# Performance work log

Hardware: AMD Instinct MI355X
Metric: run time of the kernel (lower is better)

Reference implementation:

```python
import jax, jax.numpy as jnp
import numpy as np
import math

B, S, E, H = 2, 2048, 1024, 16
D = E // H  # d_attn = 64
SCALE = 1.0 / math.sqrt(D)


def setup_inputs() -> dict:
    key = jax.random.key(0)
    ks = jax.random.split(key, 5)
    std = 0.02
    return {
        "q": jax.random.normal(ks[0], (B, S, E), dtype=jnp.float32),
        "Wq": jax.random.normal(ks[1], (E, H * D), dtype=jnp.float32) * std,
        "Wk": jax.random.normal(ks[2], (E, H * D), dtype=jnp.float32) * std,
        "Wv": jax.random.normal(ks[3], (E, H * D), dtype=jnp.float32) * std,
        "Wo": jax.random.normal(ks[4], (H * D, E), dtype=jnp.float32) * std,
        "gamma": jnp.ones((H,), dtype=jnp.float32),
    }


def reference(q, Wq, Wk, Wv, Wo, gamma):
    Bq, Sq, _ = q.shape
    # projections -> [B, H, S, D]
    qh = (q @ Wq).reshape(Bq, Sq, H, D).transpose(0, 2, 1, 3)
    kh = (q @ Wk).reshape(Bq, Sq, H, D).transpose(0, 2, 1, 3)
    vh = (q @ Wv).reshape(Bq, Sq, H, D).transpose(0, 2, 1, 3)
    # RBF distance scores: ||q||^2 - 2 q.k + ||k||^2, clamped at 0
    q_norm = jnp.sum(qh * qh, axis=-1, keepdims=True)          # [B,H,S,1]
    k_norm = jnp.sum(kh * kh, axis=-1, keepdims=True)          # [B,H,S,1]
    qk = jnp.einsum("bhsd,bhtd->bhst", qh, kh)                # [B,H,S,S]
    dist = jnp.maximum(q_norm - 2.0 * qk + jnp.swapaxes(k_norm, -2, -1), 0.0)
    scores = jnp.exp(-gamma[None, :, None, None] * SCALE * dist)
    # source: masked_fill(causal_mask == 0, 0) with mask = triu(ones, 1)
    # -> scores kept only on the STRICT upper triangle (faithful to source)
    mask = jnp.triu(jnp.ones((Sq, Sq), dtype=bool), k=1)
    scores = jnp.where(mask, scores, 0.0)
    out = jnp.einsum("bhst,bhtd->bhsd", scores, vh)            # [B,H,S,D]
    out = out.transpose(0, 2, 1, 3).reshape(Bq, Sq, H * D)
    return out @ Wo
```

## Files before the change

### kernel.cpp

```cpp
#include <hip/hip_runtime.h>
#include <stdint.h>

#define SCALE 0.125f
#define GSL_C 0.180336880111f

typedef short s16x4 __attribute__((ext_vector_type(4)));
typedef short s16x8 __attribute__((ext_vector_type(8)));
typedef float f32x4 __attribute__((ext_vector_type(4)));
typedef float f32x16 __attribute__((ext_vector_type(16)));

__device__ __forceinline__ unsigned short f2bf(float x){
  union { float f; unsigned int u; } v; v.f = x;
  unsigned int r = v.u + 0x7fffu + ((v.u >> 16) & 1u);
  return (unsigned short)(r >> 16);
}
__device__ __forceinline__ float bf2f(unsigned short u){
  union { unsigned int u; float f; } v; v.u = ((unsigned int)u) << 16;
  return v.f;
}
__device__ __forceinline__ f32x4 mfma16(s16x8 a, s16x8 b, f32x4 c){
  return __builtin_amdgcn_mfma_f32_16x16x32_bf16(a, b, c, 0, 0, 0);
}
__device__ __forceinline__ f32x16 mfma32(s16x8 a, s16x8 b, f32x16 c){
  return __builtin_amdgcn_mfma_f32_32x32x16_bf16(a, b, c, 0, 0, 0);
}
__device__ __forceinline__ void gld_lds16(const void* g, void* l){
  __builtin_amdgcn_global_load_lds(
      (const __attribute__((address_space(1))) unsigned int*)g,
      (__attribute__((address_space(3))) unsigned int*)l, 16, 0, 0);
}
__device__ __forceinline__ unsigned int cvtpk(float lo, float hi){
  unsigned int r;
  asm("v_cvt_pk_bf16_f32 %0, %1, %2" : "=v"(r) : "v"(lo), "v"(hi));
  return r;
}
__device__ __forceinline__ void plswap(unsigned int &a, unsigned int &b){
  asm("v_permlane32_swap_b32 %0, %1" : "+v"(a), "+v"(b));
}

__global__ __launch_bounds__(256) void prep_kernel(const float* __restrict__ in,
    unsigned short* __restrict__ out,
    const float* __restrict__ W0, const float* __restrict__ W1,
    const float* __restrict__ W2, const float* __restrict__ W3,
    unsigned short* __restrict__ Wt){
  int bid = blockIdx.x;
  int tid = threadIdx.x;
  if (bid < 2048){
    int i = bid*256 + tid;
    const float4* p = (const float4*)in + (size_t)i*2;
    float4 a = p[0], b = p[1];
    unsigned short t[8] = {f2bf(a.x),f2bf(a.y),f2bf(a.z),f2bf(a.w),
                           f2bf(b.x),f2bf(b.y),f2bf(b.z),f2bf(b.w)};
    *(s16x8*)(out + (size_t)i*8) = *(const s16x8*)t;
  } else {
    int idx = bid - 2048;
    int z = idx >> 8, rem = idx & 255;
    int k0 = (rem & 15)*64, n0 = (rem >> 4)*64;
    const float* src = (z==0)?W0:(z==1)?W1:(z==2)?W2:W3;
    unsigned short* dst = Wt + (size_t)z*1048576;
    __shared__ unsigned short tile[64*72];
    int r = tid>>2, c = (tid&3)*16;
    const float* p = src + (size_t)(k0+r)*1024 + n0 + c;
    #pragma unroll
    for (int j=0;j<16;j++) tile[r*72 + c + j] = f2bf(p[j]);
    __syncthreads();
    int n = tid>>2, kc = (tid&3)*16;
    unsigned short o[16];
    #pragma unroll
    for (int j=0;j<16;j++) o[j] = tile[(kc+j)*72 + n];
    *(s16x8*)&dst[(size_t)(n0+n)*1024 + k0 + kc]     = *(const s16x8*)o;
    *(s16x8*)&dst[(size_t)(n0+n)*1024 + k0 + kc + 8] = *(const s16x8*)(o+8);
  }
}

__global__ __launch_bounds__(512) void gemm_proj(const unsigned short* __restrict__ A,
    const unsigned short* __restrict__ Bt, unsigned short* __restrict__ outH,
    unsigned short* __restrict__ VtG,
    float* __restrict__ qn, float* __restrict__ kn, const float* __restrict__ gamma){
  __shared__ short As[3][4096];
  __shared__ short Bs[3][4096];
  int tid = threadIdx.x;
  int w = tid>>6, l = tid&63;
  int lm = l & 15, hi = l >> 4;
  int wr = w>>1, wc = w&1;
  int m0 = blockIdx.x*128, n0 = blockIdx.y*128;

  const unsigned short* Bz = Bt + (size_t)(n0>>10)*1048576;
  int bn0 = n0 & 1023;

  f32x4 acc[2][4];
  #pragma unroll
  for (int r=0;r<2;r++)
    #pragma unroll
    for (int c=0;c<4;c++){ f32x4 z = {0.f,0.f,0.f,0.f}; acc[r][c] = z; }

  int srow = w*16 + (l>>2);
  int schk = ((l&3) ^ ((l>>3)&3))*8;
  const unsigned short* gA = A  + (size_t)(m0  + srow)*1024 + schk;
  const unsigned short* gB = Bz + (size_t)(bn0 + srow)*1024 + schk;

  int ch = (hi ^ ((lm>>1)&3))*8;

  gld_lds16(gA,      &As[0][w*512]);
  gld_lds16(gB,      &Bs[0][w*512]);
  gld_lds16(gA + 32, &As[1][w*512]);
  gld_lds16(gB + 32, &Bs[1][w*512]);

  const int NKT = 32;
  int cur = 0;
  for (int kt=0; kt<NKT; ++kt){
    if (kt+2 < NKT){
      int wb = cur + 2; if (wb >= 3) wb -= 3;
      gld_lds16(gA + (size_t)(kt+2)*32, &As[wb][w*512]);
      gld_lds16(gB + (size_t)(kt+2)*32, &Bs[wb][w*512]);
    }
    if (kt < NKT-2)       asm volatile("s_waitcnt vmcnt(4)" ::: "memory");
    else if (kt == NKT-2) asm volatile("s_waitcnt vmcnt(2)" ::: "memory");
    else                  asm volatile("s_waitcnt vmcnt(0)" ::: "memory");
    __builtin_amdgcn_s_barrier();

    const short* cA = &As[cur][0];
    const short* cB = &Bs[cur][0];
    s16x8 af[2], bfv[4];
    #pragma unroll
    for (int r=0;r<2;r++)
      af[r]  = *(const s16x8*)(cA + (wr*32 + r*16 + lm)*32 + ch);
    #pragma unroll
    for (int c=0;c<4;c++)
      bfv[c] = *(const s16x8*)(cB + (wc*64 + c*16 + lm)*32 + ch);
    __builtin_amdgcn_s_setprio(1);
    #pragma unroll
    for (int r=0;r<2;r++)
      #pragma unroll
      for (int c=0;c<4;c++)
        acc[r][c] = mfma16(af[r], bfv[c], acc[r][c]);
    __builtin_amdgcn_s_setprio(0);
    __builtin_amdgcn_s_barrier();
    cur = (cur + 1 < 3) ? cur + 1 : 0;
  }

  int z = n0 >> 10;
  if (z == 2){
    short* tb = (w < 4) ? (&As[0][0] + w*2048) : (&Bs[0][0] + (w-4)*2048);
    #pragma unroll
    for (int r=0;r<2;r++)
      #pragma unroll
      for (int c=0;c<4;c++){
        unsigned short t4[4] = {f2bf(acc[r][c][0]), f2bf(acc[r][c][1]),
                                f2bf(acc[r][c][2]), f2bf(acc[r][c][3])};
        *(s16x4*)(tb + (c*16 + lm)*32 + r*16 + hi*4) = *(const s16x4*)t4;
      }
    int bq = m0 >> 11;
    int hq = (bn0 >> 6) + wc;
    int bh = bq*16 + hq;
    int t0w = (m0 & 2047) + wr*32;
    unsigned short* vt = VtG + (size_t)bh*131072;
    #pragma unroll
    for (int it=0; it<4; ++it){
      int d = (l>>2) + it*16;
      int tl = (l&3)*8;
      s16x8 vv = *(const s16x8*)(tb + d*32 + tl);
      *(s16x8*)(vt + (size_t)d*2048 + t0w + tl) = vv;
    }
  } else {
    unsigned short* oz = outH + (size_t)z*4194304;
    #pragma unroll
    for (int r=0;r<2;r++){
      #pragma unroll
      for (int i=0;i<4;i++){
        int m = m0 + wr*32 + r*16 + hi*4 + i;
        int bq = m >> 11, sq = m & 2047;
        float nrm = 0.f;
        #pragma unroll
        for (int c=0;c<4;c++){
          int nn = bn0 + wc*64 + c*16 + lm;
          int hq = nn >> 6, dq = nn & 63;
          int bh = bq*16 + hq;
          unsigned short bv = f2bf(acc[r][c][i]);
          oz[((size_t)bh*2048 + sq)*64 + dq] = bv;
          float vf = bf2f(bv);
          nrm = fmaf(vf, vf, nrm);
        }
        nrm += __shfl_xor(nrm, 1);
        nrm += __shfl_xor(nrm, 2);
        nrm += __shfl_xor(nrm, 4);
        nrm += __shfl_xor(nrm, 8);
        if (lm == 0){
          int hq = (bn0 + wc*64) >> 6;
          float gsl_h = gamma[hq] * GSL_C;
          float* dst = z ? kn : qn;
          dst[(size_t)(bq*16 + hq)*2048 + sq] = nrm * gsl_h;
        }
      }
    }
  }
}

__global__ __launch_bounds__(512) void gemm_out(const unsigned short* __restrict__ A,
    const unsigned short* __restrict__ Bt, float* __restrict__ outF){
  __shared__ short As[16384];
  __shared__ short Bs[8192];
  int tid = threadIdx.x;
  int w = tid>>6, l = tid&63;
  int lm = l & 15, hi = l >> 4;
  int wr = w>>1, wc = w&1;
  int m0 = blockIdx.x*128, n0 = blockIdx.y*64;

  f32x4 acc[2][2];
  #pragma unroll
  for (int r=0;r<2;r++)
    #pragma unroll
    for (int c=0;c<2;c++){ f32x4 z = {0.f,0.f,0.f,0.f}; acc[r][c] = z; }

  int rsub = l>>3, csw = ((l&7) ^ (l>>3))*8;
  const unsigned short* gA = A  + (size_t)(m0 + w*16 + rsub)*1024 + csw;
  const unsigned short* gB = Bt + (size_t)(n0 + w*8  + rsub)*1024 + csw;

  int ch0 = ((hi)     ^ (lm&7))*8;
  int ch1 = ((4 + hi) ^ (lm&7))*8;

  gld_lds16(gA,        As + w*1024);
  gld_lds16(gA + 8192, As + w*1024 + 512);
  gld_lds16(gB,        Bs + w*512);
  __syncthreads();

  const int NKT = 16;
  int buf = 0;
  for (int kt=0; kt<NKT; ++kt){
    if (kt+1 < NKT){
      const unsigned short* a = gA + (size_t)(kt+1)*64;
      const unsigned short* b = gB + (size_t)(kt+1)*64;
      gld_lds16(a,        As + (buf^1)*8192 + w*1024);
      gld_lds16(a + 8192, As + (buf^1)*8192 + w*1024 + 512);
      gld_lds16(b,        Bs + (buf^1)*4096 + w*512);
    }
    const short* curA = As + buf*8192;
    const short* curB = Bs + buf*4096;
    s16x8 af[2][2], bfv[2][2];
    #pragma unroll
    for (int r=0;r<2;r++){
      int ro = (wr*32 + r*16 + lm)*64;
      af[r][0] = *(const s16x8*)(curA + ro + ch0);
      af[r][1] = *(const s16x8*)(curA + ro + ch1);
    }
    #pragma unroll
    for (int c=0;c<2;c++){
      int ro = (wc*32 + c*16 + lm)*64;
      bfv[c][0] = *(const s16x8*)(curB + ro + ch0);
      bfv[c][1] = *(const s16x8*)(curB + ro + ch1);
    }
    __builtin_amdgcn_s_setprio(1);
    #pragma unroll
    for (int s=0;s<2;s++)
      #pragma unroll
      for (int r=0;r<2;r++)
        #pragma unroll
        for (int c=0;c<2;c++)
          acc[r][c] = mfma16(af[r][s], bfv[c][s], acc[r][c]);
    __builtin_amdgcn_s_setprio(0);
    __syncthreads();
    buf ^= 1;
  }

  #pragma unroll
  for (int r=0;r<2;r++)
    #pragma unroll
    for (int c=0;c<2;c++)
      #pragma unroll
      for (int i=0;i<4;i++){
        int m = m0 + wr*32 + r*16 + hi*4 + i;
        int n = n0 + wc*32 + c*16 + lm;
        outF[(size_t)m*1024 + n] = acc[r][c][i];
      }
}

#define JOB(si,ts,te,buf,zm) ((unsigned int)((si)|((ts)<<4)|((te)<<10)|((buf)<<16)|((zm)<<18)))
__device__ const unsigned int JOBS[32] = {
  JOB(0,0,11,0,0),   JOB(5,10,21,0,0),  JOB(0,22,32,2,0),  JOB(1,12,22,1,0),
  JOB(2,4,14,0,0),   JOB(6,22,32,1,2),  JOB(2,23,32,2,0),  JOB(7,14,23,0,0),
  JOB(0,11,22,1,0),  JOB(5,21,32,1,2),  JOB(1,2,12,0,0),   JOB(1,22,32,2,0),
  JOB(6,12,22,0,0),  JOB(2,14,23,1,0),  JOB(3,6,15,0,0),   JOB(7,23,32,1,2),
  JOB(11,22,32,0,3), JOB(3,24,32,2,0),  JOB(4,8,16,0,0),   JOB(4,16,24,1,0),
  JOB(4,24,32,2,0),  JOB(8,16,24,0,0),  JOB(3,15,24,1,0),  JOB(8,24,32,1,2),
  JOB(15,30,32,0,3), JOB(14,28,32,0,3), JOB(10,20,26,0,0), JOB(10,26,32,1,2),
  JOB(13,26,32,0,3), JOB(9,18,25,0,0),  JOB(9,25,32,1,2),  JOB(12,24,32,0,3)
};

__global__ __launch_bounds__(256, 4) void attn_kernel(const unsigned short* __restrict__ Qh,
    const unsigned short* __restrict__ Kh, const unsigned short* __restrict__ VtG,
    const float* __restrict__ qn, const float* __restrict__ kn,
    const float* __restrict__ gamma, unsigned short* __restrict__ aO0,
    unsigned short* __restrict__ aO1, unsigned short* __restrict__ aO2){
  __shared__ short Ks[2][4096];
  __shared__ short Vs[2][4096];

  int bid = blockIdx.x;
  int bh = bid & 31; int b = bh>>4, h = bh&15;
  unsigned int e = JOBS[bid >> 5];
  int si2 = e & 15, ts = (e>>4)&63, te = (e>>10)&63, bsel = (e>>16)&3, zm = (e>>18)&3;
  int s0 = si2*128;

  int tid = threadIdx.x, w = tid>>6, l = tid&63;
  int l31 = l & 31, hi5 = l >> 5, l7 = l & 7;
  float gs2l = 2.f * gamma[h] * GSL_C;

  int q0 = s0 + w*32;
  int qrow = q0 + l31;
  const unsigned short* qb = Qh + ((size_t)bh*2048 + qrow)*64;
  s16x8 qf[4];
  #pragma unroll
  for (int c=0;c<4;c++) qf[c] = *(const s16x8*)(qb + c*16 + hi5*8);
  float gq = -qn[(size_t)bh*2048 + qrow];
  const float* knp = kn + (size_t)bh*2048;

  int chs = (l7 ^ (l>>3))*8;
  const unsigned short* kp0 = Kh  + ((size_t)bh*2048 + w*8 + (l>>3))*64 + chs;
  const unsigned short* vp0 = VtG + ((size_t)bh*64 + w*8 + (l>>3))*2048 + chs;

  f32x16 accO0, accO1;
  #pragma unroll
  for (int r=0;r<16;r++){ accO0[r] = 0.f; accO1[r] = 0.f; }

#define STAGE(bufi, tabs) { \
    const unsigned short* kp = kp0 + (size_t)(tabs)*64; \
    const unsigned short* vp = vp0 + (tabs); \
    short* dK = &Ks[bufi][w*512]; \
    short* dV = &Vs[bufi][w*512]; \
    gld_lds16(kp,           dK); \
    gld_lds16(kp + 32*64,   dK + 2048); \
    gld_lds16(vp,           dV); \
    gld_lds16(vp + 32*2048, dV + 2048); \
  }

  STAGE(0, ts*64);
  __syncthreads();

  int cur = 0;
  for (int tt = ts; tt < te; ++tt, cur ^= 1){
    int t0 = tt*64;
    if (tt + 1 < te) STAGE(cur^1, (tt+1)*64);
    const short* kb = &Ks[cur][0];
    const short* vb = &Vs[cur][0];

    f32x16 sc2[2];
    #pragma unroll
    for (int tb=0; tb<2; tb++){
      int tbase = t0 + tb*32 - s0;
      if (tbase + 31 <= w*32) continue;
      f32x16 sc;
      #pragma unroll
      for (int r=0;r<16;r++) sc[r] = 0.f;
      __builtin_amdgcn_s_setprio(1);
      #pragma unroll
      for (int c=0;c<4;c++){
        s16x8 kf = *(const s16x8*)(kb + (tb*32 + l31)*64 + (((2*c + hi5) ^ l7)*8));
        sc = mfma32(kf, qf[c], sc);
      }
      __builtin_amdgcn_s_setprio(0);
      sc2[tb] = sc;
    }

    #pragma unroll
    for (int tb=0; tb<2; tb++){
      int tbase = t0 + tb*32 - s0;
      if (tbase + 31 <= w*32) continue;
      f32x16 sc = sc2[tb];
      float ev[16];
      #pragma unroll
      for (int gg=0; gg<4; gg++){
        float4 knv = *(const float4*)(knp + t0 + tb*32 + gg*8 + hi5*4);
        float ks4[4] = {knv.x, knv.y, knv.z, knv.w};
        #pragma unroll
        for (int i=0;i<4;i++){
          int r = gg*4 + i;
          ev[r] = __builtin_amdgcn_exp2f(fminf(fmaf(gs2l, sc[r], gq - ks4[i]), 0.f));
        }
      }
      if (tbase < w*32 + 32){
        #pragma unroll
        for (int r=0;r<16;r++){
          int t = t0 + tb*32 + (r&3) + 8*(r>>2) + 4*hi5;
          ev[r] = (t > qrow) ? ev[r] : 0.f;
        }
      }
      unsigned int u0 = cvtpk(ev[0],  ev[1]),  u1 = cvtpk(ev[2],  ev[3]);
      unsigned int u2 = cvtpk(ev[4],  ev[5]),  u3 = cvtpk(ev[6],  ev[7]);
      unsigned int u4 = cvtpk(ev[8],  ev[9]),  u5 = cvtpk(ev[10], ev[11]);
      unsigned int u6 = cvtpk(ev[12], ev[13]), u7 = cvtpk(ev[14], ev[15]);
      plswap(u0, u2);
      plswap(u1, u3);
      plswap(u4, u6);
      plswap(u5, u7);
      unsigned int f0[4] = {u0, u1, u2, u3};
      unsigned int f1[4] = {u4, u5, u6, u7};
      s16x8 pa0 = *(const s16x8*)f0;
      s16x8 pa1 = *(const s16x8*)f1;
      __builtin_amdgcn_s_setprio(1);
      {
        int cg0 = 2*tb, cg1 = 2*tb + 1;
        s16x8 v00 = *(const s16x8*)(vb + (l31)*64      + (((2*cg0 + hi5) ^ l7)*8));
        s16x8 v01 = *(const s16x8*)(vb + (l31)*64      + (((2*cg1 + hi5) ^ l7)*8));
        s16x8 v10 = *(const s16x8*)(vb + (32 + l31)*64 + (((2*cg0 + hi5) ^ l7)*8));
        s16x8 v11 = *(const s16x8*)(vb + (32 + l31)*64 + (((2*cg1 + hi5) ^ l7)*8));
        accO0 = mfma32(pa0, v00, accO0);
        accO0 = mfma32(pa1, v01, accO0);
        accO1 = mfma32(pa0, v10, accO1);
        accO1 = mfma32(pa1, v11, accO1);
      }
      __builtin_amdgcn_s_setprio(0);
    }
    __syncthreads();
  }
#undef STAGE

  unsigned short* aoP = (bsel==0) ? aO0 : (bsel==1) ? aO1 : aO2;
  #pragma unroll
  for (int r=0;r<16;r++){
    int s = q0 + (r&3) + 8*(r>>2) + 4*hi5;
    size_t base = ((size_t)b*2048 + s)*1024 + h*64;
    aoP[base + l31]      = f2bf(accO0[r]);
    aoP[base + 32 + l31] = f2bf(accO1[r]);
  }
  if (zm){
    s16x8 zz8 = {0,0,0,0,0,0,0,0};
    int zr = tid >> 1, zc = (tid & 1)*32;
    size_t zbase = ((size_t)b*2048 + s0 + zr)*1024 + h*64 + zc;
    if (zm & 1){
      #pragma unroll
      for (int j=0;j<4;j++) *(s16x8*)&aO1[zbase + j*8] = zz8;
    }
    if (zm & 2){
      #pragma unroll
      for (int j=0;j<4;j++) *(s16x8*)&aO2[zbase + j*8] = zz8;
    }
  }
}

__global__ __launch_bounds__(256) void sum3_kernel(unsigned short* __restrict__ a,
    const unsigned short* __restrict__ bsrc, const unsigned short* __restrict__ csrc){
  size_t i = ((size_t)blockIdx.x*256 + threadIdx.x)*8;
  s16x8 va = *(const s16x8*)(a + i);
  s16x8 vb = *(const s16x8*)(bsrc + i);
  s16x8 vc = *(const s16x8*)(csrc + i);
  unsigned short o[8];
  #pragma unroll
  for (int j=0;j<8;j++)
    o[j] = f2bf(bf2f((unsigned short)va[j]) + bf2f((unsigned short)vb[j])
                + bf2f((unsigned short)vc[j]));
  *(s16x8*)(a + i) = *(const s16x8*)o;
}

extern "C" void kernel_launch(void* const* d_in, const int* in_sizes, int n_in,
                              void* d_out, int out_size, void* d_ws, size_t ws_size,
                              hipStream_t stream){
  const float* q  = (const float*)d_in[0];
  const float* Wq = (const float*)d_in[1];
  const float* Wk = (const float*)d_in[2];
  const float* Wv = (const float*)d_in[3];
  const float* Wo = (const float*)d_in[4];
  const float* gm = (const float*)d_in[5];
  float* out = (float*)d_out;

  unsigned short* qbf = (unsigned short*)d_ws;
  unsigned short* Wt  = qbf + 4194304;
  unsigned short* Qh  = Wt  + 4194304;
  unsigned short* Kh  = Qh  + 4194304;
  unsigned short* Vh  = Kh  + 4194304;
  unsigned short* Vt  = Vh  + 4194304;
  unsigned short* aO  = Vt  + 4194304;
  float* qn = (float*)(aO + 4194304);
  float* kn = qn + 65536;

  unsigned short* aO1 = qbf;
  unsigned short* aO2 = Vh;

  prep_kernel  <<<dim3(3072), 256, 0, stream>>>(q, qbf, Wq, Wk, Wv, Wo, Wt);
  gemm_proj    <<<dim3(32,24), 512, 0, stream>>>(qbf, Wt, Qh, Vt, qn, kn, gm);
  attn_kernel  <<<dim3(1024), 256, 0, stream>>>(Qh, Kh, Vt, qn, kn, gm, aO, aO1, aO2);
  sum3_kernel  <<<dim3(2048), 256, 0, stream>>>(aO, aO1, aO2);
  gemm_out     <<<dim3(32,16), 512, 0, stream>>>(aO, Wt + 3*1048576, out);
}
```

Before: 100.6 us.

## Triple-buffer output projection GEMM with explicit vmcnt waits

Converts the output-projection GEMM from double to triple buffering in LDS. Global-to-LDS loads run two K-tiles ahead, and the full __syncthreads is replaced by explicit s_waitcnt vmcnt counts plus raw barriers. The aim is to hide more global-load latency behind the MFMA work. In exchange it uses more LDS, and correctness now depends on the hand-counted vmcnt values matching the number of outstanding loads.

```diff
diff --git a/kernel.cpp b/kernel.cpp
--- a/kernel.cpp
+++ b/kernel.cpp
@@ -198,8 +198,8 @@
 
 __global__ __launch_bounds__(512) void gemm_out(const unsigned short* __restrict__ A,
     const unsigned short* __restrict__ Bt, float* __restrict__ outF){
-  __shared__ short As[16384];
-  __shared__ short Bs[8192];
+  __shared__ short As[3][8192];
+  __shared__ short Bs[3][4096];
   int tid = threadIdx.x;
   int w = tid>>6, l = tid&63;
   int lm = l & 15, hi = l >> 4;
@@ -219,23 +219,31 @@
   int ch0 = ((hi)     ^ (lm&7))*8;
   int ch1 = ((4 + hi) ^ (lm&7))*8;
 
-  gld_lds16(gA,        As + w*1024);
-  gld_lds16(gA + 8192, As + w*1024 + 512);
-  gld_lds16(gB,        Bs + w*512);
-  __syncthreads();
+  gld_lds16(gA,             &As[0][w*1024]);
+  gld_lds16(gA + 8192,      &As[0][w*1024 + 512]);
+  gld_lds16(gB,             &Bs[0][w*512]);
+  gld_lds16(gA + 64,        &As[1][w*1024]);
+  gld_lds16(gA + 8192 + 64, &As[1][w*1024 + 512]);
+  gld_lds16(gB + 64,        &Bs[1][w*512]);
 
   const int NKT = 16;
-  int buf = 0;
+  int cur = 0;
   for (int kt=0; kt<NKT; ++kt){
-    if (kt+1 < NKT){
-      const unsigned short* a = gA + (size_t)(kt+1)*64;
-      const unsigned short* b = gB + (size_t)(kt+1)*64;
-      gld_lds16(a,        As + (buf^1)*8192 + w*1024);
-      gld_lds16(a + 8192, As + (buf^1)*8192 + w*1024 + 512);
-      gld_lds16(b,        Bs + (buf^1)*4096 + w*512);
-    }
-    const short* curA = As + buf*8192;
-    const short* curB = Bs + buf*4096;
+    if (kt+2 < NKT){
+      int wb = cur + 2; if (wb >= 3) wb -= 3;
+      const unsigned short* a = gA + (size_t)(kt+2)*64;
+      const unsigned short* b = gB + (size_t)(kt+2)*64;
+      gld_lds16(a,        &As[wb][w*1024]);
+      gld_lds16(a + 8192, &As[wb][w*1024 + 512]);
+      gld_lds16(b,        &Bs[wb][w*512]);
+    }
+    if (kt < NKT-2)       asm volatile("s_waitcnt vmcnt(6)" ::: "memory");
+    else if (kt == NKT-2) asm volatile("s_waitcnt vmcnt(3)" ::: "memory");
+    else                  asm volatile("s_waitcnt vmcnt(0)" ::: "memory");
+    __builtin_amdgcn_s_barrier();
+
+    const short* curA = &As[cur][0];
+    const short* curB = &Bs[cur][0];
     s16x8 af[2][2], bfv[2][2];
     #pragma unroll
     for (int r=0;r<2;r++){
@@ -258,8 +266,8 @@
         for (int c=0;c<2;c++)
           acc[r][c] = mfma16(af[r][s], bfv[c][s], acc[r][c]);
     __builtin_amdgcn_s_setprio(0);
-    __syncthreads();
-    buf ^= 1;
+    __builtin_amdgcn_s_barrier();
+    cur = (cur + 1 < 3) ? cur + 1 : 0;
   }
 
   #pragma unroll
```

Result: no change. 100.0 us, median of 2 (-0.6%).
